# Optimization experiments

Hardware: AMD Instinct MI355X
Metric: run time of the kernel (lower is better)

The kernel has to match this reference:

```python
import jax, jax.numpy as jnp
import numpy as np
from jax import lax

# dims per init_kwargs / input_specs
V, D, N, W, B, T = 32000, 512, 250000, 64, 4, 1024
LOOPS, THRESH = 4, 0.99


def _ln(x, scale, bias):
    m = jnp.mean(x, -1, keepdims=True)
    v = jnp.var(x, -1, keepdims=True)
    return (x - m) * lax.rsqrt(v + 1e-5) * scale + bias


def setup_inputs() -> dict:
    key = jax.random.key(0)
    ks = jax.random.split(key, 12)
    s = 0.02
    p = lambda k, shape: jax.random.normal(k, shape, jnp.float32) * s
    return {
        "input_ids": jax.random.randint(ks[0], (B, T), 0, V),
        "embed": p(ks[1], (V, D)),
        "enc_w": p(ks[2], (D, D)), "enc_b": jnp.zeros((D,), jnp.float32),
        "ln_enc_s": jnp.ones((D,), jnp.float32), "ln_enc_b": jnp.zeros((D,), jnp.float32),
        "idx_w": p(ks[3], (D, D)), "idx_b": jnp.zeros((D,), jnp.float32),
        "mu_w": p(ks[4], (D, 1)), "mu_b": jnp.zeros((1,), jnp.float32),
        "sig_w": p(ks[5], (D, 1)), "sig_b": jnp.zeros((1,), jnp.float32),
        "pool_table": p(ks[6], (N, D)),
        "int_w1": p(ks[7], (2 * D, D)), "int_b1": jnp.zeros((D,), jnp.float32),
        "int_w2": p(ks[8], (D, D)), "int_b2": jnp.zeros((D,), jnp.float32),
        "ln_s": jnp.ones((D,), jnp.float32), "ln_b": jnp.zeros((D,), jnp.float32),
        "halt_w": p(ks[9], (D, 1)), "halt_b": jnp.zeros((1,), jnp.float32),
        "dec_w": p(ks[10], (D, V)), "dec_b": jnp.zeros((V,), jnp.float32),
    }


def reference(input_ids, embed, enc_w, enc_b, ln_enc_s, ln_enc_b,
              idx_w, idx_b, mu_w, mu_b, sig_w, sig_b, pool_table,
              int_w1, int_b1, int_w2, int_b2, ln_s, ln_b,
              halt_w, halt_b, dec_w, dec_b):
    # TinyController.encode: embed -> Dense -> gelu -> LayerNorm
    hidden = _ln(jax.nn.gelu(embed[input_ids] @ enc_w + enc_b), ln_enc_s, ln_enc_b)  # [B,T,D]
    state = hidden
    dt = hidden.dtype
    halt_prob = jnp.zeros((B, T, 1), dt)
    halted = jnp.zeros((B, T, 1), dt)
    idxs = []
    for _ in range(LOOPS):  # fixed small loop count, unrolled
        prev = state
        pooled = jnp.mean(state, axis=1)                       # [B,D]
        h = jax.nn.gelu(pooled @ idx_w + idx_b)
        mu = jax.nn.sigmoid(h @ mu_w + mu_b)                   # [B,1], coord in [0,1]
        sigma = jax.nn.softplus(h @ sig_w + sig_b) + 1e-4      # [B,1]
        # CoordinateMassivePool: contiguous window of W rows around mu*N
        center = mu[:, 0] * N
        start = jnp.clip(jnp.floor(center - W / 2).astype(jnp.int32), 0, N - W)  # [B]
        window = jax.vmap(lambda s: lax.dynamic_slice(pool_table, (s, 0), (W, D)))(start)  # [B,W,D]
        pos = (start[:, None] + jnp.arange(W)[None, :]).astype(dt) / N            # [B,W]
        w = jnp.exp(-0.5 * ((pos - mu) / sigma) ** 2)
        w = w / jnp.sum(w, axis=-1, keepdims=True)
        retrieved = jnp.einsum('bw,bwd->bd', w, window)        # [B,D]
        combined = jnp.concatenate(
            [state, jnp.broadcast_to(retrieved[:, None, :], (B, T, D))], axis=-1)  # [B,T,2D]
        integrated = _ln(jax.nn.gelu(combined @ int_w1 + int_b1) @ int_w2 + int_b2, ln_s, ln_b)
        candidate = state + integrated
        # ACT halting
        p_halt = jax.nn.sigmoid(candidate @ halt_w + halt_b)   # [B,T,1]
        halt_prob = halt_prob + p_halt * (1.0 - halted)
        new_halted = (halt_prob > THRESH).astype(dt)
        state = (1.0 - halted) * candidate + halted * prev
        halted = new_halted
        idxs.append(start)
    logits = state @ dec_w + dec_b                             # [B,T,V]
    all_indices = jnp.stack(idxs, axis=1)                      # [B,LOOPS]
    return logits, all_indices
```

## Files before the change

### kernel.cpp

```cpp
#include <hip/hip_runtime.h>

#define DEV __device__ __forceinline__

typedef __attribute__((ext_vector_type(8))) short bf16x8;
typedef __attribute__((ext_vector_type(4))) float f32x4;

typedef const __attribute__((address_space(1))) void* gsrc_t;
typedef __attribute__((address_space(3))) void* gdst_t;

DEV void gld16(const void* g, void* l){ __builtin_amdgcn_global_load_lds((gsrc_t)g,(gdst_t)l,16,0,0); }
DEV void gld4 (const void* g, void* l){ __builtin_amdgcn_global_load_lds((gsrc_t)g,(gdst_t)l, 4,0,0); }

DEV unsigned short f2bf(float f){
  union { float f; unsigned int u; } x; x.f = f;
  unsigned int u = x.u;
  return (unsigned short)((u + 0x7fffu + ((u >> 16) & 1u)) >> 16);
}
DEV unsigned long long pack4bf(float a, float b, float c, float d){
  return (unsigned long long)f2bf(a)
       | ((unsigned long long)f2bf(b) << 16)
       | ((unsigned long long)f2bf(c) << 32)
       | ((unsigned long long)f2bf(d) << 48);
}
DEV float gelu_t(float x){
  float u = 0.7978845608028654f * (x + 0.044715f * x * x * x);
  return 0.5f * x * (1.0f + tanhf(u));
}
DEV float sigmoidf_(float x){ return 1.0f / (1.0f + expf(-x)); }

DEV void BAR_TOP(){ __builtin_amdgcn_s_barrier(); asm volatile("" ::: "memory"); }
DEV void BAR_END(){
  __builtin_amdgcn_sched_barrier(0);
  asm volatile("s_waitcnt lgkmcnt(0)" ::: "memory");
  __builtin_amdgcn_s_barrier();
  asm volatile("" ::: "memory");
}

__global__ __launch_bounds__(256) void kTdec(const float* __restrict__ W,
                                             unsigned short* __restrict__ out){
  __shared__ float t[64][65];
  int n0 = blockIdx.x * 64, k0 = blockIdx.y * 64;
  int tid = threadIdx.x;
  #pragma unroll
  for (int i = 0; i < 16; i++){
    int idx = i * 256 + tid; int r = idx >> 6, c = idx & 63;
    t[r][c] = W[(size_t)(k0 + r) * 32000 + n0 + c];
  }
  __syncthreads();
  #pragma unroll
  for (int i = 0; i < 16; i++){
    int idx = i * 256 + tid; int r = idx >> 6, c = idx & 63;
    out[(size_t)(n0 + r) * 512 + k0 + c] = f2bf(t[c][r]);
  }
}

__global__ __launch_bounds__(256) void kT3(const float* __restrict__ s0, const float* __restrict__ s1,
                                           const float* __restrict__ s2,
                                           unsigned short* __restrict__ d0, unsigned short* __restrict__ d1,
                                           unsigned short* __restrict__ d2){
  __shared__ float t[64][65];
  int z = blockIdx.z;
  const float* W = (z == 0) ? s0 : (z == 1) ? s1 : s2;
  unsigned short* D = (z == 0) ? d0 : (z == 1) ? d1 : d2;
  int n0 = blockIdx.x * 64, k0 = blockIdx.y * 64;
  int tid = threadIdx.x;
  #pragma unroll
  for (int i = 0; i < 16; i++){
    int idx = i * 256 + tid; int r = idx >> 6, c = idx & 63;
    t[r][c] = W[(size_t)(k0 + r) * 512 + n0 + c];
  }
  __syncthreads();
  #pragma unroll
  for (int i = 0; i < 16; i++){
    int idx = i * 256 + tid; int r = idx >> 6, c = idx & 63;
    D[(size_t)(n0 + r) * 512 + k0 + c] = f2bf(t[c][r]);
  }
}

__global__ __launch_bounds__(128) void kGather(const int* __restrict__ ids,
                                               const float* __restrict__ embed,
                                               unsigned short* __restrict__ E){
  int row = blockIdx.x, tid = threadIdx.x;
  int id = ids[row];
  float4 v = ((const float4*)(embed + (size_t)id * 512))[tid];
  *(unsigned long long*)(E + (size_t)row * 512 + tid * 4) = pack4bf(v.x, v.y, v.z, v.w);
}

template<int ENC>
__global__ __launch_bounds__(512) void kGemmLN(
    const unsigned short* __restrict__ A, const unsigned short* __restrict__ BT,
    const float* __restrict__ bias, const float* __restrict__ lns, const float* __restrict__ lnb,
    const float* __restrict__ hw, const float* __restrict__ hb,
    float* __restrict__ st, unsigned short* __restrict__ stb,
    float* __restrict__ part, float* __restrict__ halt_p, float* __restrict__ halted){
  __shared__ alignas(16) unsigned short lA[2][32 * 32];
  __shared__ alignas(16) unsigned short lB[2][512 * 32];
  __shared__ float pS[8][32], pQ[8][32], pH[8][32];
  __shared__ float sMean[32], sRs[32], sFac[32];
  const int tid = threadIdx.x, w = tid >> 6, lane = tid & 63;
  const int q = lane >> 4, c = lane & 15, lk8 = q * 8;
  const int r0 = blockIdx.x * 32;
  const int ar = tid >> 4, ak = (tid & 15) * 2;
  const int br = tid >> 2, bk = (tid & 3) * 8;
  f32x4 acc[2][4] = {};

  auto STAGE = [&](int buf, int k0){
    gld4 (A  + (size_t)(r0 + ar) * 512 + k0 + ak, &lA[buf][ar * 32 + ak]);
    #pragma unroll
    for (int i = 0; i < 4; i++)
      gld16(BT + (size_t)(i * 128 + br) * 512 + k0 + bk, &lB[buf][(i * 512 + tid) * 8]);
  };

  STAGE(0, 0);
  #pragma unroll
  for (int t = 0; t < 16; t++){
    if (t < 15){
      STAGE((t + 1) & 1, (t + 1) * 32);
      asm volatile("s_waitcnt vmcnt(5)" ::: "memory");
    } else {
      asm volatile("s_waitcnt vmcnt(0)" ::: "memory");
    }
    BAR_TOP();
    const unsigned short* la = lA[t & 1];
    const unsigned short* lb = lB[t & 1];
    bf16x8 af[2], bfv[4];
    #pragma unroll
    for (int m = 0; m < 2; m++) af[m]  = *(const bf16x8*)&la[(m * 16 + c) * 32 + lk8];
    #pragma unroll
    for (int n = 0; n < 4; n++) bfv[n] = *(const bf16x8*)&lb[(w * 64 + n * 16 + c) * 32 + lk8];
    #pragma unroll
    for (int m = 0; m < 2; m++)
      #pragma unroll
      for (int n = 0; n < 4; n++)
        acc[m][n] = __builtin_amdgcn_mfma_f32_16x16x32_bf16(af[m], bfv[n], acc[m][n], 0, 0, 0);
    BAR_END();
  }

  #pragma unroll
  for (int n = 0; n < 4; n++){
    float bcol = bias[w * 64 + n * 16 + c];
    #pragma unroll
    for (int m = 0; m < 2; m++)
      #pragma unroll
      for (int r = 0; r < 4; r++){
        float v = acc[m][n][r] + bcol;
        if (ENC) v = gelu_t(v);
        acc[m][n][r] = v;
      }
  }
  float rS[2][4], rQ[2][4];
  #pragma unroll
  for (int m = 0; m < 2; m++)
    #pragma unroll
    for (int r = 0; r < 4; r++){
      float s = 0.f, s2 = 0.f;
      #pragma unroll
      for (int n = 0; n < 4; n++){ float v = acc[m][n][r]; s += v; s2 += v * v; }
      rS[m][r] = s; rQ[m][r] = s2;
    }
  #pragma unroll
  for (int mask = 1; mask < 16; mask <<= 1)
    #pragma unroll
    for (int m = 0; m < 2; m++)
      #pragma unroll
      for (int r = 0; r < 4; r++){
        rS[m][r] += __shfl_xor(rS[m][r], mask);
        rQ[m][r] += __shfl_xor(rQ[m][r], mask);
      }
  if (c == 0)
    #pragma unroll
    for (int m = 0; m < 2; m++)
      #pragma unroll
      for (int r = 0; r < 4; r++){
        pS[w][m * 16 + q * 4 + r] = rS[m][r];
        pQ[w][m * 16 + q * 4 + r] = rQ[m][r];
      }
  __syncthreads();
  if (tid < 32){
    float s = 0.f, s2 = 0.f;
    #pragma unroll
    for (int v = 0; v < 8; v++){ s += pS[v][tid]; s2 += pQ[v][tid]; }
    float mean = s * (1.f / 512.f);
    float var  = s2 * (1.f / 512.f) - mean * mean;
    sMean[tid] = mean; sRs[tid] = rsqrtf(var + 1e-5f);
    if (ENC){ halt_p[r0 + tid] = 0.f; halted[r0 + tid] = 0.f; }
  }
  __syncthreads();
  float lnsv[4], lnbv[4];
  #pragma unroll
  for (int n = 0; n < 4; n++){ lnsv[n] = lns[w * 64 + n * 16 + c]; lnbv[n] = lnb[w * 64 + n * 16 + c]; }
  #pragma unroll
  for (int m = 0; m < 2; m++)
    #pragma unroll
    for (int r = 0; r < 4; r++){
      int row = m * 16 + q * 4 + r;
      float mu = sMean[row], rs = sRs[row];
      #pragma unroll
      for (int n = 0; n < 4; n++)
        acc[m][n][r] = (acc[m][n][r] - mu) * rs * lnsv[n] + lnbv[n];
    }

  float sold[2][4][4];
  if (!ENC){
    float hwv[4];
    #pragma unroll
    for (int n = 0; n < 4; n++) hwv[n] = hw[w * 64 + n * 16 + c];
    #pragma unroll
    for (int m = 0; m < 2; m++)
      #pragma unroll
      for (int r = 0; r < 4; r++){
        int row = m * 16 + q * 4 + r;
        #pragma unroll
        for (int n = 0; n < 4; n++)
          sold[m][n][r] = st[(size_t)(r0 + row) * 512 + w * 64 + n * 16 + c];
      }
    float rH[2][4];
    #pragma unroll
    for (int m = 0; m < 2; m++)
      #pragma unroll
      for (int r = 0; r < 4; r++){
        float d = 0.f;
        #pragma unroll
        for (int n = 0; n < 4; n++) d += (sold[m][n][r] + acc[m][n][r]) * hwv[n];
        rH[m][r] = d;
      }
    #pragma unroll
    for (int mask = 1; mask < 16; mask <<= 1)
      #pragma unroll
      for (int m = 0; m < 2; m++)
        #pragma unroll
        for (int r = 0; r < 4; r++) rH[m][r] += __shfl_xor(rH[m][r], mask);
    if (c == 0)
      #pragma unroll
      for (int m = 0; m < 2; m++)
        #pragma unroll
        for (int r = 0; r < 4; r++) pH[w][m * 16 + q * 4 + r] = rH[m][r];
    __syncthreads();
    if (tid < 32){
      float d = 0.f;
      #pragma unroll
      for (int v = 0; v < 8; v++) d += pH[v][tid];
      float hd = halted[r0 + tid];
      float p  = sigmoidf_(d + hb[0]);
      float hp = halt_p[r0 + tid] + p * (1.f - hd);
      halt_p[r0 + tid] = hp;
      halted[r0 + tid] = (hp > 0.99f) ? 1.f : 0.f;
      sFac[tid] = 1.f - hd;
    }
    __syncthreads();
    #pragma unroll
    for (int m = 0; m < 2; m++)
      #pragma unroll
      for (int r = 0; r < 4; r++){
        int row = m * 16 + q * 4 + r;
        float f = sFac[row];
        #pragma unroll
        for (int n = 0; n < 4; n++)
          acc[m][n][r] = sold[m][n][r] + f * acc[m][n][r];
      }
  }

  #pragma unroll
  for (int m = 0; m < 2; m++)
    #pragma unroll
    for (int r = 0; r < 4; r++){
      int row = r0 + m * 16 + q * 4 + r;
      #pragma unroll
      for (int n = 0; n < 4; n++){
        int col = w * 64 + n * 16 + c;
        float v = acc[m][n][r];
        st [(size_t)row * 512 + col] = v;
        stb[(size_t)row * 512 + col] = f2bf(v);
      }
    }
  #pragma unroll
  for (int n = 0; n < 4; n++){
    float s = 0.f;
    #pragma unroll
    for (int m = 0; m < 2; m++)
      #pragma unroll
      for (int r = 0; r < 4; r++) s += acc[m][n][r];
    s += __shfl_xor(s, 16);
    s += __shfl_xor(s, 32);
    if (q == 0) part[(size_t)blockIdx.x * 512 + w * 64 + n * 16 + c] = s;
  }
}

__global__ __launch_bounds__(256) void kGemm64(const unsigned short* __restrict__ A,
                                               const unsigned short* __restrict__ BT,
                                               const float* __restrict__ rb,
                                               unsigned short* __restrict__ C){
  __shared__ alignas(16) unsigned short lA[2][64 * 32];
  __shared__ alignas(16) unsigned short lB[2][64 * 32];
  const int tid = threadIdx.x, w = tid >> 6, lane = tid & 63;
  const int q = lane >> 4, c = lane & 15, lk8 = q * 8;
  const int wm = w >> 1, wn = w & 1;
  const int m0 = blockIdx.y * 64, n0 = blockIdx.x * 64;
  const int sr = tid >> 2, sk = (tid & 3) * 8;
  f32x4 acc[2][2] = {};

  auto STAGE = [&](int buf, int k0){
    gld16(A  + (size_t)(m0 + sr) * 512 + k0 + sk, &lA[buf][tid * 8]);
    gld16(BT + (size_t)(n0 + sr) * 512 + k0 + sk, &lB[buf][tid * 8]);
  };

  STAGE(0, 0);
  #pragma unroll
  for (int t = 0; t < 16; t++){
    if (t < 15){
      STAGE((t + 1) & 1, (t + 1) * 32);
      asm volatile("s_waitcnt vmcnt(2)" ::: "memory");
    } else {
      asm volatile("s_waitcnt vmcnt(0)" ::: "memory");
    }
    BAR_TOP();
    bf16x8 af[2], bfv[2];
    #pragma unroll
    for (int m = 0; m < 2; m++) af[m]  = *(const bf16x8*)&lA[t & 1][(wm * 32 + m * 16 + c) * 32 + lk8];
    #pragma unroll
    for (int n = 0; n < 2; n++) bfv[n] = *(const bf16x8*)&lB[t & 1][(wn * 32 + n * 16 + c) * 32 + lk8];
    #pragma unroll
    for (int m = 0; m < 2; m++)
      #pragma unroll
      for (int n = 0; n < 2; n++)
        acc[m][n] = __builtin_amdgcn_mfma_f32_16x16x32_bf16(af[m], bfv[n], acc[m][n], 0, 0, 0);
    BAR_END();
  }

  #pragma unroll
  for (int m = 0; m < 2; m++)
    #pragma unroll
    for (int n = 0; n < 2; n++)
      #pragma unroll
      for (int r = 0; r < 4; r++){
        int row = m0 + wm * 32 + m * 16 + q * 4 + r;
        int col = n0 + wn * 32 + n * 16 + c;
        float v = acc[m][n][r] + rb[((row >> 10) << 9) + col];
        C[(size_t)row * 512 + col] = f2bf(gelu_t(v));
      }
}

__global__ __launch_bounds__(256) void kGemmDec(const unsigned short* __restrict__ A,
                                                const unsigned short* __restrict__ BT,
                                                const float* __restrict__ bias,
                                                float* __restrict__ C){
  __shared__ alignas(16) unsigned short lA[2][128 * 32];
  __shared__ alignas(16) unsigned short lB[2][128 * 32];
  const int tid = threadIdx.x, w = tid >> 6, lane = tid & 63;
  const int wm = w >> 1, wn = w & 1;
  const int c = lane & 15, q = lane >> 4, lk = q * 8;
  int flat = blockIdx.x;
  flat = (flat & 7) * 1000 + (flat >> 3);
  const int m0 = (flat & 31) * 128;
  const int n0 = (flat >> 5) * 128;
  const int srow = tid >> 2, sch = (tid & 3) * 8;
  f32x4 acc[4][4] = {};

  auto STAGE = [&](int buf, int k0){
    gld16(A  + (size_t)(m0 + srow) * 512 + k0 + sch,      &lA[buf][srow * 32 + sch]);
    gld16(A  + (size_t)(m0 + 64 + srow) * 512 + k0 + sch, &lA[buf][(64 + srow) * 32 + sch]);
    gld16(BT + (size_t)(n0 + srow) * 512 + k0 + sch,      &lB[buf][srow * 32 + sch]);
    gld16(BT + (size_t)(n0 + 64 + srow) * 512 + k0 + sch, &lB[buf][(64 + srow) * 32 + sch]);
  };

  STAGE(0, 0);
  #pragma unroll
  for (int t = 0; t < 16; t++){
    if (t < 15){
      STAGE((t + 1) & 1, (t + 1) * 32);
      asm volatile("s_waitcnt vmcnt(4)" ::: "memory");
    } else {
      asm volatile("s_waitcnt vmcnt(0)" ::: "memory");
    }
    BAR_TOP();
    const unsigned short* la = lA[t & 1];
    const unsigned short* lb = lB[t & 1];
    bf16x8 af[4], bfr[4];
    #pragma unroll
    for (int m = 0; m < 4; m++) af[m]  = *(const bf16x8*)&la[(wm * 64 + m * 16 + c) * 32 + lk];
    #pragma unroll
    for (int n = 0; n < 4; n++) bfr[n] = *(const bf16x8*)&lb[(wn * 64 + n * 16 + c) * 32 + lk];
    #pragma unroll
    for (int m = 0; m < 4; m++)
      #pragma unroll
      for (int n = 0; n < 4; n++)
        acc[m][n] = __builtin_amdgcn_mfma_f32_16x16x32_bf16(af[m], bfr[n], acc[m][n], 0, 0, 0);
    BAR_END();
  }

  #pragma unroll
  for (int m = 0; m < 4; m++){
    int rbase = m0 + wm * 64 + m * 16 + q * 4;
    #pragma unroll
    for (int n = 0; n < 4; n++){
      int col = n0 + wn * 64 + n * 16 + c;
      float bcol = bias[col];
      #pragma unroll
      for (int r = 0; r < 4; r++)
        __builtin_nontemporal_store(acc[m][n][r] + bcol,
                                    &C[(size_t)(rbase + r) * 32000 + col]);
    }
  }
}

__global__ __launch_bounds__(512) void kCtl(const float* __restrict__ part,
                                            const float* __restrict__ idx_w, const float* __restrict__ idx_b,
                                            const float* __restrict__ mu_w, const float* __restrict__ mu_b,
                                            const float* __restrict__ sig_w, const float* __restrict__ sig_b,
                                            const float* __restrict__ pool_table,
                                            const float* __restrict__ w1b, const float* __restrict__ int_b1,
                                            float* __restrict__ r2, float* __restrict__ outIdx, int loop){
  __shared__ float xs[512];
  __shared__ float red[512];
  __shared__ float red2[512];
  __shared__ float evals[64];
  __shared__ float sc[4];
  int b = blockIdx.x, tid = threadIdx.x;

  float s = 0.f;
  #pragma unroll 8
  for (int c2 = 0; c2 < 32; c2++) s += part[(size_t)(b * 32 + c2) * 512 + tid];
  xs[tid] = s * (1.0f / 1024.0f);
  __syncthreads();

  float a = idx_b[tid];
  #pragma unroll 16
  for (int i = 0; i < 512; i++)
    a = fmaf(xs[i], idx_w[(size_t)i * 512 + tid], a);
  float hv = gelu_t(a);
  red[tid]  = hv * mu_w[tid];
  red2[tid] = hv * sig_w[tid];
  __syncthreads();
  for (int off2 = 256; off2 > 0; off2 >>= 1){
    if (tid < off2){ red[tid] += red[tid + off2]; red2[tid] += red2[tid + off2]; }
    __syncthreads();
  }
  if (tid == 0){
    float mu = sigmoidf_(red[0] + mu_b[0]);
    float sg = log1pf(expf(red2[0] + sig_b[0])) + 1e-4f;
    float center = mu * 250000.0f;
    int stt = (int)floorf(center - 32.0f);
    stt = stt < 0 ? 0 : (stt > 250000 - 64 ? 250000 - 64 : stt);
    sc[0] = mu; sc[1] = sg; sc[2] = (float)stt;
    outIdx[b * 4 + loop] = (float)stt;
  }
  __syncthreads();
  if (tid < 64){
    float pos = (sc[2] + (float)tid) * (1.0f / 250000.0f);
    float z = (pos - sc[0]) / sc[1];
    evals[tid] = expf(-0.5f * z * z);
  }
  __syncthreads();
  if (tid == 0){
    float wsum = 0.f;
    for (int j = 0; j < 64; j++) wsum += evals[j];
    sc[3] = wsum;
  }
  __syncthreads();
  int stt = (int)sc[2];
  float r = 0.f;
  #pragma unroll 8
  for (int j = 0; j < 64; j++)
    r = fmaf(evals[j], pool_table[(size_t)(stt + j) * 512 + tid], r);
  r /= sc[3];
  __syncthreads();
  xs[tid] = r;
  __syncthreads();
  float a2 = int_b1[tid];
  #pragma unroll 16
  for (int i = 0; i < 512; i++)
    a2 = fmaf(xs[i], w1b[(size_t)i * 512 + tid], a2);
  r2[(size_t)b * 512 + tid] = a2;
}

extern "C" void kernel_launch(void* const* d_in, const int* in_sizes, int n_in,
                              void* d_out, int out_size, void* d_ws, size_t ws_size,
                              hipStream_t stream){
  (void)in_sizes; (void)n_in; (void)out_size; (void)ws_size;
  const int*   ids    = (const int*)  d_in[0];
  const float* embed  = (const float*)d_in[1];
  const float* enc_w  = (const float*)d_in[2];
  const float* enc_b  = (const float*)d_in[3];
  const float* ln_es  = (const float*)d_in[4];
  const float* ln_eb  = (const float*)d_in[5];
  const float* idx_w  = (const float*)d_in[6];
  const float* idx_b  = (const float*)d_in[7];
  const float* mu_w   = (const float*)d_in[8];
  const float* mu_b   = (const float*)d_in[9];
  const float* sig_w  = (const float*)d_in[10];
  const float* sig_b  = (const float*)d_in[11];
  const float* pool_t = (const float*)d_in[12];
  const float* int_w1 = (const float*)d_in[13];
  const float* int_b1 = (const float*)d_in[14];
  const float* int_w2 = (const float*)d_in[15];
  const float* int_b2 = (const float*)d_in[16];
  const float* ln_s   = (const float*)d_in[17];
  const float* ln_b   = (const float*)d_in[18];
  const float* halt_w = (const float*)d_in[19];
  const float* halt_b = (const float*)d_in[20];
  const float* dec_w  = (const float*)d_in[21];
  const float* dec_b  = (const float*)d_in[22];

  char* ws = (char*)d_ws;
  size_t off = 0;
  auto alloc = [&](size_t bytes)->char*{
    char* p = ws + off; off += (bytes + 255) & ~(size_t)255; return p;
  };
  unsigned short* dec_wT  = (unsigned short*)alloc(32000ull * 512 * 2);
  unsigned short* enc_wT  = (unsigned short*)alloc(512ull * 512 * 2);
  unsigned short* w1T     = (unsigned short*)alloc(512ull * 512 * 2);
  unsigned short* w2T     = (unsigned short*)alloc(512ull * 512 * 2);
  unsigned short* bufB    = (unsigned short*)alloc(4096ull * 512 * 2);
  float*          state   = (float*)alloc(4096ull * 512 * 4);
  unsigned short* state_b = (unsigned short*)alloc(4096ull * 512 * 2);
  float*          part    = (float*)alloc(128ull * 512 * 4);
  float*          r2      = (float*)alloc(4ull * 512 * 4);
  float*          halt_p  = (float*)alloc(4096 * 4);
  float*          halted  = (float*)alloc(4096 * 4);
  float*          outF    = (float*)d_out;

  hipLaunchKernelGGL(kTdec, dim3(500, 8), dim3(256), 0, stream, dec_w, dec_wT);
  hipLaunchKernelGGL(kT3, dim3(8, 8, 3), dim3(256), 0, stream,
                     enc_w, int_w1, int_w2, enc_wT, w1T, w2T);

  hipLaunchKernelGGL(kGather, dim3(4096), dim3(128), 0, stream, ids, embed, bufB);
  hipLaunchKernelGGL((kGemmLN<1>), dim3(128), dim3(512), 0, stream,
                     bufB, enc_wT, enc_b, ln_es, ln_eb,
                     (const float*)nullptr, (const float*)nullptr,
                     state, state_b, part, halt_p, halted);

  for (int l = 0; l < 4; l++){
    hipLaunchKernelGGL(kCtl, dim3(4), dim3(512), 0, stream, part, idx_w, idx_b,
                       mu_w, mu_b, sig_w, sig_b, pool_t,
                       int_w1 + 512 * 512, int_b1,
                       r2, outF + 131072000, l);
    hipLaunchKernelGGL(kGemm64, dim3(8, 64), dim3(256), 0, stream,
                       state_b, w1T, r2, bufB);
    hipLaunchKernelGGL((kGemmLN<0>), dim3(128), dim3(512), 0, stream,
                       bufB, w2T, int_b2, ln_s, ln_b, halt_w, halt_b,
                       state, state_b, part, halt_p, halted);
  }

  hipLaunchKernelGGL(kGemmDec, dim3(8000), dim3(256), 0, stream,
                     state_b, dec_wT, dec_b, (float*)d_out);
}
```

Before: 524.9 us.

## Merge prep kernels and fuse controller into GemmLN tail via last-block atomic

Folds the three preprocessing kernels (decoder weight transpose, small weight transposes, embedding gather) into one launch. It also removes the separate controller kernel: each GemmLN block bumps a per-batch atomic counter, and the last of the 32 blocks for that batch computes the pooled mean, mu/sigma, window retrieval and the r2 projection, reusing the LDS staging buffer. This cuts kernel launches and inter-kernel gaps on the serial loop chain. In exchange it adds threadfence/atomic overhead, and the controller work now runs on a single tail block per batch at the end of the GEMM.

```diff
diff --git a/kernel.cpp b/kernel.cpp
--- a/kernel.cpp
+++ b/kernel.cpp
@@ -36,70 +36,157 @@
   asm volatile("" ::: "memory");
 }
 
-__global__ __launch_bounds__(256) void kTdec(const float* __restrict__ W,
-                                             unsigned short* __restrict__ out){
+__global__ __launch_bounds__(256) void kPrep(const float* __restrict__ dec_w,
+                                             unsigned short* __restrict__ dec_wT,
+                                             const float* __restrict__ s0, const float* __restrict__ s1,
+                                             const float* __restrict__ s2,
+                                             unsigned short* __restrict__ d0, unsigned short* __restrict__ d1,
+                                             unsigned short* __restrict__ d2,
+                                             const int* __restrict__ ids,
+                                             const float* __restrict__ embed,
+                                             unsigned short* __restrict__ E,
+                                             unsigned int* __restrict__ cnt){
   __shared__ float t[64][65];
-  int n0 = blockIdx.x * 64, k0 = blockIdx.y * 64;
-  int tid = threadIdx.x;
-  #pragma unroll
-  for (int i = 0; i < 16; i++){
-    int idx = i * 256 + tid; int r = idx >> 6, c = idx & 63;
-    t[r][c] = W[(size_t)(k0 + r) * 32000 + n0 + c];
-  }
-  __syncthreads();
-  #pragma unroll
-  for (int i = 0; i < 16; i++){
-    int idx = i * 256 + tid; int r = idx >> 6, c = idx & 63;
-    out[(size_t)(n0 + r) * 512 + k0 + c] = f2bf(t[c][r]);
-  }
-}
-
-__global__ __launch_bounds__(256) void kT3(const float* __restrict__ s0, const float* __restrict__ s1,
-                                           const float* __restrict__ s2,
-                                           unsigned short* __restrict__ d0, unsigned short* __restrict__ d1,
-                                           unsigned short* __restrict__ d2){
-  __shared__ float t[64][65];
-  int z = blockIdx.z;
-  const float* W = (z == 0) ? s0 : (z == 1) ? s1 : s2;
-  unsigned short* D = (z == 0) ? d0 : (z == 1) ? d1 : d2;
-  int n0 = blockIdx.x * 64, k0 = blockIdx.y * 64;
-  int tid = threadIdx.x;
-  #pragma unroll
-  for (int i = 0; i < 16; i++){
-    int idx = i * 256 + tid; int r = idx >> 6, c = idx & 63;
-    t[r][c] = W[(size_t)(k0 + r) * 512 + n0 + c];
-  }
-  __syncthreads();
-  #pragma unroll
-  for (int i = 0; i < 16; i++){
-    int idx = i * 256 + tid; int r = idx >> 6, c = idx & 63;
-    D[(size_t)(n0 + r) * 512 + k0 + c] = f2bf(t[c][r]);
-  }
-}
-
-__global__ __launch_bounds__(128) void kGather(const int* __restrict__ ids,
-                                               const float* __restrict__ embed,
-                                               unsigned short* __restrict__ E){
-  int row = blockIdx.x, tid = threadIdx.x;
-  int id = ids[row];
-  float4 v = ((const float4*)(embed + (size_t)id * 512))[tid];
-  *(unsigned long long*)(E + (size_t)row * 512 + tid * 4) = pack4bf(v.x, v.y, v.z, v.w);
-}
-
-template<int ENC>
+  const int bid = blockIdx.x, tid = threadIdx.x;
+  if (bid == 0 && tid < 16) cnt[tid] = 0u;
+  if (bid < 4000){
+    int n0 = (bid % 500) * 64, k0 = (bid / 500) * 64;
+    #pragma unroll
+    for (int i = 0; i < 16; i++){
+      int idx = i * 256 + tid; int r = idx >> 6, c = idx & 63;
+      t[r][c] = dec_w[(size_t)(k0 + r) * 32000 + n0 + c];
+    }
+    __syncthreads();
+    #pragma unroll
+    for (int i = 0; i < 16; i++){
+      int idx = i * 256 + tid; int r = idx >> 6, c = idx & 63;
+      dec_wT[(size_t)(n0 + r) * 512 + k0 + c] = f2bf(t[c][r]);
+    }
+  } else if (bid < 4192){
+    int rel = bid - 4000;
+    int z = rel >> 6, rem = rel & 63;
+    const float* W = (z == 0) ? s0 : (z == 1) ? s1 : s2;
+    unsigned short* D = (z == 0) ? d0 : (z == 1) ? d1 : d2;
+    int n0 = (rem & 7) * 64, k0 = (rem >> 3) * 64;
+    #pragma unroll
+    for (int i = 0; i < 16; i++){
+      int idx = i * 256 + tid; int r = idx >> 6, c = idx & 63;
+      t[r][c] = W[(size_t)(k0 + r) * 512 + n0 + c];
+    }
+    __syncthreads();
+    #pragma unroll
+    for (int i = 0; i < 16; i++){
+      int idx = i * 256 + tid; int r = idx >> 6, c = idx & 63;
+      D[(size_t)(n0 + r) * 512 + k0 + c] = f2bf(t[c][r]);
+    }
+  } else {
+    int idx = bid - 4192;
+    int row = idx * 2 + (tid >> 7);
+    int t2  = tid & 127;
+    int id = ids[row];
+    float4 v = ((const float4*)(embed + (size_t)id * 512))[t2];
+    *(unsigned long long*)(E + (size_t)row * 512 + t2 * 4) = pack4bf(v.x, v.y, v.z, v.w);
+  }
+}
+
+DEV void ctl_tail(int b, int tid, unsigned int* cnt, int slot,
+                  const float* part,
+                  const float* idx_w, const float* idx_b,
+                  const float* mu_w, const float* mu_b,
+                  const float* sig_w, const float* sig_b,
+                  const float* pool_table,
+                  const float* w1b, const float* int_b1,
+                  float* r2, float* outIdx, int nextloop,
+                  float* cs, unsigned int* sLast){
+  float* xs   = cs;
+  float* red  = cs + 512;
+  float* red2 = cs + 1024;
+  float* ev   = cs + 1536;
+  float* sc   = cs + 1600;
+  __threadfence();
+  __syncthreads();
+  if (tid == 0) *sLast = atomicAdd(&cnt[slot * 4 + b], 1u);
+  __syncthreads();
+  if (*sLast != 31u) return;
+  __threadfence();
+  float s = 0.f;
+  #pragma unroll 8
+  for (int c2 = 0; c2 < 32; c2++) s += part[(size_t)(b * 32 + c2) * 512 + tid];
+  xs[tid] = s * (1.0f / 1024.0f);
+  __syncthreads();
+  float a = idx_b[tid];
+  #pragma unroll 16
+  for (int i = 0; i < 512; i++)
+    a = fmaf(xs[i], idx_w[(size_t)i * 512 + tid], a);
+  float hv = gelu_t(a);
+  red[tid]  = hv * mu_w[tid];
+  red2[tid] = hv * sig_w[tid];
+  __syncthreads();
+  for (int off2 = 256; off2 > 0; off2 >>= 1){
+    if (tid < off2){ red[tid] += red[tid + off2]; red2[tid] += red2[tid + off2]; }
+    __syncthreads();
+  }
+  if (tid == 0){
+    float mu = sigmoidf_(red[0] + mu_b[0]);
+    float sg = log1pf(expf(red2[0] + sig_b[0])) + 1e-4f;
+    float center = mu * 250000.0f;
+    int stt = (int)floorf(center - 32.0f);
+    stt = stt < 0 ? 0 : (stt > 250000 - 64 ? 250000 - 64 : stt);
+    sc[0] = mu; sc[1] = sg; sc[2] = (float)stt;
+    outIdx[b * 4 + nextloop] = (float)stt;
+  }
+  __syncthreads();
+  if (tid < 64){
+    float pos = (sc[2] + (float)tid) * (1.0f / 250000.0f);
+    float z = (pos - sc[0]) / sc[1];
+    ev[tid] = expf(-0.5f * z * z);
+  }
+  __syncthreads();
+  if (tid == 0){
+    float ws = 0.f;
+    for (int j = 0; j < 64; j++) ws += ev[j];
+    sc[3] = ws;
+  }
+  __syncthreads();
+  int stt = (int)sc[2];
+  float r = 0.f;
+  #pragma unroll 8
+  for (int j = 0; j < 64; j++)
+    r = fmaf(ev[j], pool_table[(size_t)(stt + j) * 512 + tid], r);
+  r /= sc[3];
+  __syncthreads();
+  xs[tid] = r;
+  __syncthreads();
+  float a2 = int_b1[tid];
+  #pragma unroll 16
+  for (int i = 0; i < 512; i++)
+    a2 = fmaf(xs[i], w1b[(size_t)i * 512 + tid], a2);
+  r2[(size_t)b * 512 + tid] = a2;
+}
+
+template<int ENC, int TAIL>
 __global__ __launch_bounds__(512) void kGemmLN(
     const unsigned short* __restrict__ A, const unsigned short* __restrict__ BT,
     const float* __restrict__ bias, const float* __restrict__ lns, const float* __restrict__ lnb,
     const float* __restrict__ hw, const float* __restrict__ hb,
     float* __restrict__ st, unsigned short* __restrict__ stb,
-    float* __restrict__ part, float* __restrict__ halt_p, float* __restrict__ halted){
+    float* __restrict__ part, float* __restrict__ halt_p, float* __restrict__ halted,
+    unsigned int* __restrict__ cnt, int slot,
+    const float* __restrict__ idx_w, const float* __restrict__ idx_b,
+    const float* __restrict__ mu_w, const float* __restrict__ mu_b,
+    const float* __restrict__ sig_w, const float* __restrict__ sig_b,
+    const float* __restrict__ pool_table,
+    const float* __restrict__ w1b, const float* __restrict__ int_b1,
+    float* __restrict__ r2, float* __restrict__ outIdx, int nextloop){
   __shared__ alignas(16) unsigned short lA[2][32 * 32];
   __shared__ alignas(16) unsigned short lB[2][512 * 32];
   __shared__ float pS[8][32], pQ[8][32], pH[8][32];
   __shared__ float sMean[32], sRs[32], sFac[32];
+  __shared__ unsigned int sLast;
   const int tid = threadIdx.x, w = tid >> 6, lane = tid & 63;
   const int q = lane >> 4, c = lane & 15, lk8 = q * 8;
   const int r0 = blockIdx.x * 32;
+  const int b = blockIdx.x >> 5;
   const int ar = tid >> 4, ak = (tid & 15) * 2;
   const int br = tid >> 2, bk = (tid & 3) * 8;
   f32x4 acc[2][4] = {};
@@ -283,6 +370,11 @@
     s += __shfl_xor(s, 16);
     s += __shfl_xor(s, 32);
     if (q == 0) part[(size_t)blockIdx.x * 512 + w * 64 + n * 16 + c] = s;
+  }
+  if (TAIL){
+    ctl_tail(b, tid, cnt, slot, part, idx_w, idx_b, mu_w, mu_b, sig_w, sig_b,
+             pool_table, w1b, int_b1, r2, outIdx, nextloop,
+             (float*)&lB[0][0], &sLast);
   }
 }
 
@@ -401,76 +493,6 @@
                                     &C[(size_t)(rbase + r) * 32000 + col]);
     }
   }
-}
-
-__global__ __launch_bounds__(512) void kCtl(const float* __restrict__ part,
-                                            const float* __restrict__ idx_w, const float* __restrict__ idx_b,
-                                            const float* __restrict__ mu_w, const float* __restrict__ mu_b,
-                                            const float* __restrict__ sig_w, const float* __restrict__ sig_b,
-                                            const float* __restrict__ pool_table,
-                                            const float* __restrict__ w1b, const float* __restrict__ int_b1,
-                                            float* __restrict__ r2, float* __restrict__ outIdx, int loop){
-  __shared__ float xs[512];
-  __shared__ float red[512];
-  __shared__ float red2[512];
-  __shared__ float evals[64];
-  __shared__ float sc[4];
-  int b = blockIdx.x, tid = threadIdx.x;
-
-  float s = 0.f;
-  #pragma unroll 8
-  for (int c2 = 0; c2 < 32; c2++) s += part[(size_t)(b * 32 + c2) * 512 + tid];
-  xs[tid] = s * (1.0f / 1024.0f);
-  __syncthreads();
-
-  float a = idx_b[tid];
-  #pragma unroll 16
-  for (int i = 0; i < 512; i++)
-    a = fmaf(xs[i], idx_w[(size_t)i * 512 + tid], a);
-  float hv = gelu_t(a);
-  red[tid]  = hv * mu_w[tid];
-  red2[tid] = hv * sig_w[tid];
-  __syncthreads();
-  for (int off2 = 256; off2 > 0; off2 >>= 1){
-    if (tid < off2){ red[tid] += red[tid + off2]; red2[tid] += red2[tid + off2]; }
-    __syncthreads();
-  }
-  if (tid == 0){
-    float mu = sigmoidf_(red[0] + mu_b[0]);
-    float sg = log1pf(expf(red2[0] + sig_b[0])) + 1e-4f;
-    float center = mu * 250000.0f;
-    int stt = (int)floorf(center - 32.0f);
-    stt = stt < 0 ? 0 : (stt > 250000 - 64 ? 250000 - 64 : stt);
-    sc[0] = mu; sc[1] = sg; sc[2] = (float)stt;
-    outIdx[b * 4 + loop] = (float)stt;
-  }
-  __syncthreads();
-  if (tid < 64){
-    float pos = (sc[2] + (float)tid) * (1.0f / 250000.0f);
-    float z = (pos - sc[0]) / sc[1];
-    evals[tid] = expf(-0.5f * z * z);
-  }
-  __syncthreads();
-  if (tid == 0){
-    float wsum = 0.f;
-    for (int j = 0; j < 64; j++) wsum += evals[j];
-    sc[3] = wsum;
-  }
-  __syncthreads();
-  int stt = (int)sc[2];
-  float r = 0.f;
-  #pragma unroll 8
-  for (int j = 0; j < 64; j++)
-    r = fmaf(evals[j], pool_table[(size_t)(stt + j) * 512 + tid], r);
-  r /= sc[3];
-  __syncthreads();
-  xs[tid] = r;
-  __syncthreads();
-  float a2 = int_b1[tid];
-  #pragma unroll 16
-  for (int i = 0; i < 512; i++)
-    a2 = fmaf(xs[i], w1b[(size_t)i * 512 + tid], a2);
-  r2[(size_t)b * 512 + tid] = a2;
 }
 
 extern "C" void kernel_launch(void* const* d_in, const int* in_sizes, int n_in,
@@ -517,28 +539,37 @@
   float*          r2      = (float*)alloc(4ull * 512 * 4);
   float*          halt_p  = (float*)alloc(4096 * 4);
   float*          halted  = (float*)alloc(4096 * 4);
+  unsigned int*   cnt     = (unsigned int*)alloc(16 * 4);
   float*          outF    = (float*)d_out;
-
-  hipLaunchKernelGGL(kTdec, dim3(500, 8), dim3(256), 0, stream, dec_w, dec_wT);
-  hipLaunchKernelGGL(kT3, dim3(8, 8, 3), dim3(256), 0, stream,
-                     enc_w, int_w1, int_w2, enc_wT, w1T, w2T);
-
-  hipLaunchKernelGGL(kGather, dim3(4096), dim3(128), 0, stream, ids, embed, bufB);
-  hipLaunchKernelGGL((kGemmLN<1>), dim3(128), dim3(512), 0, stream,
+  const float*    w1b     = int_w1 + 512 * 512;
+
+  hipLaunchKernelGGL(kPrep, dim3(6240), dim3(256), 0, stream,
+                     dec_w, dec_wT, enc_w, int_w1, int_w2, enc_wT, w1T, w2T,
+                     ids, embed, bufB, cnt);
+
+  hipLaunchKernelGGL((kGemmLN<1, 1>), dim3(128), dim3(512), 0, stream,
                      bufB, enc_wT, enc_b, ln_es, ln_eb,
                      (const float*)nullptr, (const float*)nullptr,
-                     state, state_b, part, halt_p, halted);
+                     state, state_b, part, halt_p, halted,
+                     cnt, 0, idx_w, idx_b, mu_w, mu_b, sig_w, sig_b, pool_t,
+                     w1b, int_b1, r2, outF + 131072000, 0);
 
   for (int l = 0; l < 4; l++){
-    hipLaunchKernelGGL(kCtl, dim3(4), dim3(512), 0, stream, part, idx_w, idx_b,
-                       mu_w, mu_b, sig_w, sig_b, pool_t,
-                       int_w1 + 512 * 512, int_b1,
-                       r2, outF + 131072000, l);
     hipLaunchKernelGGL(kGemm64, dim3(8, 64), dim3(256), 0, stream,
                        state_b, w1T, r2, bufB);
-    hipLaunchKernelGGL((kGemmLN<0>), dim3(128), dim3(512), 0, stream,
-                       bufB, w2T, int_b2, ln_s, ln_b, halt_w, halt_b,
-                       state, state_b, part, halt_p, halted);
+    if (l < 3){
+      hipLaunchKernelGGL((kGemmLN<0, 1>), dim3(128), dim3(512), 0, stream,
+                         bufB, w2T, int_b2, ln_s, ln_b, halt_w, halt_b,
+                         state, state_b, part, halt_p, halted,
+                         cnt, l + 1, idx_w, idx_b, mu_w, mu_b, sig_w, sig_b, pool_t,
+                         w1b, int_b1, r2, outF + 131072000, l + 1);
+    } else {
+      hipLaunchKernelGGL((kGemmLN<0, 0>), dim3(128), dim3(512), 0, stream,
+                         bufB, w2T, int_b2, ln_s, ln_b, halt_w, halt_b,
+                         state, state_b, part, halt_p, halted,
+                         cnt, 0, idx_w, idx_b, mu_w, mu_b, sig_w, sig_b, pool_t,
+                         w1b, int_b1, r2, outF + 131072000, 0);
+    }
   }
 
   hipLaunchKernelGGL(kGemmDec, dim3(8000), dim3(256), 0, stream,
```

Measured after the change: 644.0 us. 22.7% more time.

## Merge prep kernels and deepen decoder GEMM pipeline with swizzled LDS

Applied to the files above, without the earlier changes.

Folds the decoder-weight transpose, the three small weight transposes and the embedding gather into one launch that branches on block index, removing two kernel launches. The decoder GEMM now stages 64-wide K chunks as two 32-wide sub-buffers with double buffering. It issues the next global-to-LDS loads after reading fragments, so global fetches overlap the MFMA work. An XOR swizzle on the k offset is meant to cut LDS bank conflicts, and s_setprio raises priority around the MFMA block; the deeper buffering doubles LDS use, which may lower occupancy.

```diff
diff --git a/kernel.cpp b/kernel.cpp
--- a/kernel.cpp
+++ b/kernel.cpp
@@ -36,54 +36,55 @@
   asm volatile("" ::: "memory");
 }
 
-__global__ __launch_bounds__(256) void kTdec(const float* __restrict__ W,
-                                             unsigned short* __restrict__ out){
+__global__ __launch_bounds__(256) void kPrep(const float* __restrict__ dec_w,
+                                             unsigned short* __restrict__ dec_wT,
+                                             const float* __restrict__ s0, const float* __restrict__ s1,
+                                             const float* __restrict__ s2,
+                                             unsigned short* __restrict__ d0, unsigned short* __restrict__ d1,
+                                             unsigned short* __restrict__ d2,
+                                             const int* __restrict__ ids,
+                                             const float* __restrict__ embed,
+                                             unsigned short* __restrict__ E){
   __shared__ float t[64][65];
-  int n0 = blockIdx.x * 64, k0 = blockIdx.y * 64;
-  int tid = threadIdx.x;
-  #pragma unroll
-  for (int i = 0; i < 16; i++){
-    int idx = i * 256 + tid; int r = idx >> 6, c = idx & 63;
-    t[r][c] = W[(size_t)(k0 + r) * 32000 + n0 + c];
-  }
-  __syncthreads();
-  #pragma unroll
-  for (int i = 0; i < 16; i++){
-    int idx = i * 256 + tid; int r = idx >> 6, c = idx & 63;
-    out[(size_t)(n0 + r) * 512 + k0 + c] = f2bf(t[c][r]);
-  }
-}
-
-__global__ __launch_bounds__(256) void kT3(const float* __restrict__ s0, const float* __restrict__ s1,
-                                           const float* __restrict__ s2,
-                                           unsigned short* __restrict__ d0, unsigned short* __restrict__ d1,
-                                           unsigned short* __restrict__ d2){
-  __shared__ float t[64][65];
-  int z = blockIdx.z;
-  const float* W = (z == 0) ? s0 : (z == 1) ? s1 : s2;
-  unsigned short* D = (z == 0) ? d0 : (z == 1) ? d1 : d2;
-  int n0 = blockIdx.x * 64, k0 = blockIdx.y * 64;
-  int tid = threadIdx.x;
-  #pragma unroll
-  for (int i = 0; i < 16; i++){
-    int idx = i * 256 + tid; int r = idx >> 6, c = idx & 63;
-    t[r][c] = W[(size_t)(k0 + r) * 512 + n0 + c];
-  }
-  __syncthreads();
-  #pragma unroll
-  for (int i = 0; i < 16; i++){
-    int idx = i * 256 + tid; int r = idx >> 6, c = idx & 63;
-    D[(size_t)(n0 + r) * 512 + k0 + c] = f2bf(t[c][r]);
-  }
-}
-
-__global__ __launch_bounds__(128) void kGather(const int* __restrict__ ids,
-                                               const float* __restrict__ embed,
-                                               unsigned short* __restrict__ E){
-  int row = blockIdx.x, tid = threadIdx.x;
-  int id = ids[row];
-  float4 v = ((const float4*)(embed + (size_t)id * 512))[tid];
-  *(unsigned long long*)(E + (size_t)row * 512 + tid * 4) = pack4bf(v.x, v.y, v.z, v.w);
+  const int bid = blockIdx.x, tid = threadIdx.x;
+  if (bid < 4000){
+    int n0 = (bid % 500) * 64, k0 = (bid / 500) * 64;
+    #pragma unroll
+    for (int i = 0; i < 16; i++){
+      int idx = i * 256 + tid; int r = idx >> 6, c = idx & 63;
+      t[r][c] = dec_w[(size_t)(k0 + r) * 32000 + n0 + c];
+    }
+    __syncthreads();
+    #pragma unroll
+    for (int i = 0; i < 16; i++){
+      int idx = i * 256 + tid; int r = idx >> 6, c = idx & 63;
+      dec_wT[(size_t)(n0 + r) * 512 + k0 + c] = f2bf(t[c][r]);
+    }
+  } else if (bid < 4192){
+    int rel = bid - 4000;
+    int z = rel >> 6, rem = rel & 63;
+    const float* W = (z == 0) ? s0 : (z == 1) ? s1 : s2;
+    unsigned short* D = (z == 0) ? d0 : (z == 1) ? d1 : d2;
+    int n0 = (rem & 7) * 64, k0 = (rem >> 3) * 64;
+    #pragma unroll
+    for (int i = 0; i < 16; i++){
+      int idx = i * 256 + tid; int r = idx >> 6, c = idx & 63;
+      t[r][c] = W[(size_t)(k0 + r) * 512 + n0 + c];
+    }
+    __syncthreads();
+    #pragma unroll
+    for (int i = 0; i < 16; i++){
+      int idx = i * 256 + tid; int r = idx >> 6, c = idx & 63;
+      D[(size_t)(n0 + r) * 512 + k0 + c] = f2bf(t[c][r]);
+    }
+  } else {
+    int idx = bid - 4192;
+    int row = idx * 2 + (tid >> 7);
+    int t2  = tid & 127;
+    int id = ids[row];
+    float4 v = ((const float4*)(embed + (size_t)id * 512))[t2];
+    *(unsigned long long*)(E + (size_t)row * 512 + t2 * 4) = pack4bf(v.x, v.y, v.z, v.w);
+  }
 }
 
 template<int ENC>
@@ -344,60 +345,73 @@
                                                 const unsigned short* __restrict__ BT,
                                                 const float* __restrict__ bias,
                                                 float* __restrict__ C){
-  __shared__ alignas(16) unsigned short lA[2][128 * 32];
-  __shared__ alignas(16) unsigned short lB[2][128 * 32];
+  __shared__ alignas(16) unsigned short lA[2][2][128 * 32];
+  __shared__ alignas(16) unsigned short lB[2][2][128 * 32];
   const int tid = threadIdx.x, w = tid >> 6, lane = tid & 63;
   const int wm = w >> 1, wn = w & 1;
-  const int c = lane & 15, q = lane >> 4, lk = q * 8;
+  const int c = lane & 15, q = lane >> 4;
+  const int rk8 = (q ^ ((c >> 1) & 3)) * 8;
   int flat = blockIdx.x;
   flat = (flat & 7) * 1000 + (flat >> 3);
   const int m0 = (flat & 31) * 128;
   const int n0 = (flat >> 5) * 128;
-  const int srow = tid >> 2, sch = (tid & 3) * 8;
+  const int srow  = tid >> 2;
+  const int skoff = ((tid & 3) ^ ((srow >> 1) & 3)) * 8;
+  const int sdst  = srow * 32 + (tid & 3) * 8;
   f32x4 acc[4][4] = {};
 
-  auto STAGE = [&](int buf, int k0){
-    gld16(A  + (size_t)(m0 + srow) * 512 + k0 + sch,      &lA[buf][srow * 32 + sch]);
-    gld16(A  + (size_t)(m0 + 64 + srow) * 512 + k0 + sch, &lA[buf][(64 + srow) * 32 + sch]);
-    gld16(BT + (size_t)(n0 + srow) * 512 + k0 + sch,      &lB[buf][srow * 32 + sch]);
-    gld16(BT + (size_t)(n0 + 64 + srow) * 512 + k0 + sch, &lB[buf][(64 + srow) * 32 + sch]);
+  auto STG = [&](const unsigned short* M, unsigned short* dst, int base, int k0s){
+    gld16(M + (size_t)(base + srow) * 512 + k0s + skoff, dst + sdst);
+    gld16(M + (size_t)(base + 64 + srow) * 512 + k0s + skoff, dst + 64 * 32 + sdst);
   };
 
-  STAGE(0, 0);
-  #pragma unroll
-  for (int t = 0; t < 16; t++){
-    if (t < 15){
-      STAGE((t + 1) & 1, (t + 1) * 32);
-      asm volatile("s_waitcnt vmcnt(4)" ::: "memory");
-    } else {
-      asm volatile("s_waitcnt vmcnt(0)" ::: "memory");
-    }
-    BAR_TOP();
-    const unsigned short* la = lA[t & 1];
-    const unsigned short* lb = lB[t & 1];
-    bf16x8 af[4], bfr[4];
-    #pragma unroll
-    for (int m = 0; m < 4; m++) af[m]  = *(const bf16x8*)&la[(wm * 64 + m * 16 + c) * 32 + lk];
-    #pragma unroll
-    for (int n = 0; n < 4; n++) bfr[n] = *(const bf16x8*)&lb[(wn * 64 + n * 16 + c) * 32 + lk];
-    #pragma unroll
-    for (int m = 0; m < 4; m++)
-      #pragma unroll
-      for (int n = 0; n < 4; n++)
-        acc[m][n] = __builtin_amdgcn_mfma_f32_16x16x32_bf16(af[m], bfr[n], acc[m][n], 0, 0, 0);
-    BAR_END();
-  }
-
-  #pragma unroll
-  for (int m = 0; m < 4; m++){
-    int rbase = m0 + wm * 64 + m * 16 + q * 4;
-    #pragma unroll
-    for (int n = 0; n < 4; n++){
-      int col = n0 + wn * 64 + n * 16 + c;
+  STG(A,  &lA[0][0][0], m0, 0);
+  STG(BT, &lB[0][0][0], n0, 0);
+  STG(A,  &lA[0][1][0], m0, 32);
+  STG(BT, &lB[0][1][0], n0, 32);
+
+  for (int t = 0; t < 8; t++){
+    const int buf = t & 1, nbuf = buf ^ 1;
+    const int nk0 = (t + 1) * 64;
+    #pragma unroll
+    for (int s = 0; s < 2; s++){
+      if (t == 7 && s == 1) asm volatile("s_waitcnt vmcnt(0)" ::: "memory");
+      else                  asm volatile("s_waitcnt vmcnt(4)" ::: "memory");
+      __builtin_amdgcn_s_barrier();
+      asm volatile("" ::: "memory");
+      bf16x8 af[4], bfr[4];
+      #pragma unroll
+      for (int mf = 0; mf < 4; mf++)
+        af[mf] = *(const bf16x8*)&lA[buf][s][(wm * 64 + mf * 16 + c) * 32 + rk8];
+      #pragma unroll
+      for (int nf = 0; nf < 4; nf++)
+        bfr[nf] = *(const bf16x8*)&lB[buf][s][(wn * 64 + nf * 16 + c) * 32 + rk8];
+      if (t < 7){
+        STG(A,  &lA[nbuf][s][0], m0, nk0 + s * 32);
+        STG(BT, &lB[nbuf][s][0], n0, nk0 + s * 32);
+      }
+      asm volatile("s_waitcnt lgkmcnt(0)" ::: "memory");
+      __builtin_amdgcn_sched_barrier(0);
+      __builtin_amdgcn_s_setprio(1);
+      #pragma unroll
+      for (int mf = 0; mf < 4; mf++)
+        #pragma unroll
+        for (int nf = 0; nf < 4; nf++)
+          acc[mf][nf] = __builtin_amdgcn_mfma_f32_16x16x32_bf16(af[mf], bfr[nf], acc[mf][nf], 0, 0, 0);
+      __builtin_amdgcn_s_setprio(0);
+    }
+  }
+
+  #pragma unroll
+  for (int mf = 0; mf < 4; mf++){
+    int rbase = m0 + wm * 64 + mf * 16 + q * 4;
+    #pragma unroll
+    for (int nf = 0; nf < 4; nf++){
+      int col = n0 + wn * 64 + nf * 16 + c;
       float bcol = bias[col];
       #pragma unroll
       for (int r = 0; r < 4; r++)
-        __builtin_nontemporal_store(acc[m][n][r] + bcol,
+        __builtin_nontemporal_store(acc[mf][nf][r] + bcol,
                                     &C[(size_t)(rbase + r) * 32000 + col]);
     }
   }
@@ -519,11 +533,10 @@
   float*          halted  = (float*)alloc(4096 * 4);
   float*          outF    = (float*)d_out;
 
-  hipLaunchKernelGGL(kTdec, dim3(500, 8), dim3(256), 0, stream, dec_w, dec_wT);
-  hipLaunchKernelGGL(kT3, dim3(8, 8, 3), dim3(256), 0, stream,
-                     enc_w, int_w1, int_w2, enc_wT, w1T, w2T);
-
-  hipLaunchKernelGGL(kGather, dim3(4096), dim3(128), 0, stream, ids, embed, bufB);
+  hipLaunchKernelGGL(kPrep, dim3(6240), dim3(256), 0, stream,
+                     dec_w, dec_wT, enc_w, int_w1, int_w2, enc_wT, w1T, w2T,
+                     ids, embed, bufB);
+
   hipLaunchKernelGGL((kGemmLN<1>), dim3(128), dim3(512), 0, stream,
                      bufB, enc_wT, enc_b, ln_es, ln_eb,
                      (const float*)nullptr, (const float*)nullptr,
```

Result: no change. 528.0 us (+0.6%).
